# Performance work log

Hardware: AMD Instinct MI355X
Metric: run time of the kernel (lower is better)

The kernel has to match this reference:

```python
import jax, jax.numpy as jnp
import numpy as np

EPS = 1e-5


def _whiten(X, T):
    # X: (B, C, H, W); group whitening with g=1, d=C, m=B*H*W
    B, C, H, W = X.shape
    g, d = 1, C
    x = jnp.transpose(X, (1, 0, 2, 3)).reshape(g, d, -1)  # (g, d, m)
    m = x.shape[-1]
    mean = jnp.mean(x, axis=-1, keepdims=True)
    xc = x - mean
    I = jnp.broadcast_to(jnp.eye(d, dtype=X.dtype)[None], (g, d, d))
    Sigma = EPS * I + jnp.einsum('gim,gjm->gij', xc, xc) / m
    rTr = 1.0 / jnp.trace(Sigma, axis1=1, axis2=2)[:, None, None]  # 1/tr(Sigma)
    Sigma_N = Sigma * rTr
    P = I
    for _ in range(T):  # Newton-Schulz: P <- 1.5*P - 0.5*P^3 @ Sigma_N
        P = 1.5 * P - 0.5 * (P @ P @ P @ Sigma_N)
    wm = P * jnp.sqrt(rTr)  # inverse sqrt of Sigma
    xn = jnp.einsum('gij,gjm->gim', wm, xc)  # (g, d, m)
    return jnp.transpose(xn.reshape(C, B, H, W), (1, 0, 2, 3))


def reference(X, rot, T):
    # mode = -1: whiten then rotate with running_rot, affine=False
    B, C, H, W = X.shape
    g = rot.shape[0]
    d = C // g
    Xn = _whiten(X, T)                       # (B, C, H, W)
    Xh = Xn.reshape(B, g, d, H, W)
    Xr = jnp.einsum('bgchw,gdc->bgdhw', Xh, rot)
    return Xr.reshape(B, C, H, W)


def setup_inputs() -> dict:
    key = jax.random.key(0)
    k1, k2 = jax.random.split(key)
    X = jax.random.normal(k1, (32, 512, 56, 56), dtype=jnp.float32)
    # running_rot buffer; use a random orthogonal matrix for realism
    A = jax.random.normal(k2, (512, 512), dtype=jnp.float32)
    Q, _ = jnp.linalg.qr(A)
    rot = Q[None]  # (1, 512, 512)
    return {"X": X, "rot": rot, "T": 10}
```

## Files before the change

kernel.cpp:

```cpp
#include <hip/hip_runtime.h>
#include <hip/hip_bf16.h>

typedef __bf16 v8bf __attribute__((ext_vector_type(8)));
typedef float  v4f  __attribute__((ext_vector_type(4)));
typedef unsigned short u16;
typedef unsigned int   u32;

#define GAS __attribute__((address_space(1)))
#define LAS __attribute__((address_space(3)))

constexpr int C_ = 512;
constexpr int S_ = 3136;
constexpr int B_ = 32;
constexpr int M_ = B_ * S_;
constexpr float INV_M = 1.0f / (float)M_;

__device__ __forceinline__ void async16(const u16* g, u16* l) {
  __builtin_amdgcn_global_load_lds((const GAS u32*)g, (LAS u32*)l, 16, 0, 0);
}

__device__ __forceinline__ u16 f2bf(float f) {
  u32 u = __builtin_bit_cast(u32, f);
  u += 0x7fffu + ((u >> 16) & 1u);
  return (u16)(u >> 16);
}

__global__ __launch_bounds__(256) void prep_kernel(const float* __restrict__ X,
        u16* __restrict__ xbf, u16* __restrict__ xbfT, float* __restrict__ chsum) {
  __shared__ u16 Ts[64 * 65];
  const int tid = threadIdx.x;
  const int s0 = blockIdx.x * 64;
  const int c0 = blockIdx.y * 64;
  const int b  = blockIdx.z;

  const int i  = tid >> 2;
  const int jc = (tid & 3) * 16;
  const float* xp = X + (b * C_ + c0 + i) * S_ + s0 + jc;
  u16* op = xbf + (c0 + i) * M_ + b * S_ + s0 + jc;
  float ssum = 0.f;
  #pragma unroll
  for (int u = 0; u < 4; ++u) {
    float4 xv = *(const float4*)(xp + u * 4);
    ssum += xv.x + xv.y + xv.z + xv.w;
    u16 e0 = f2bf(xv.x), e1 = f2bf(xv.y), e2 = f2bf(xv.z), e3 = f2bf(xv.w);
    *(ushort4*)(op + u * 4) = make_ushort4(e0, e1, e2, e3);
    const int lb = i * 65 + jc + u * 4;
    Ts[lb + 0] = e0; Ts[lb + 1] = e1; Ts[lb + 2] = e2; Ts[lb + 3] = e3;
  }
  ssum += __shfl_down(ssum, 2, 4);
  ssum += __shfl_down(ssum, 1, 4);
  if ((tid & 3) == 0) atomicAdd(&chsum[c0 + i], ssum);
  __syncthreads();

  const int lane = tid & 63, wv = tid >> 6;
  #pragma unroll
  for (int p = 0; p < 2; ++p) {
    const int j  = p * 32 + wv * 8 + (lane >> 3);
    const int cc = (lane & 7) * 8;
    u16 tmp[8];
    #pragma unroll
    for (int e = 0; e < 8; ++e) tmp[e] = Ts[(cc + e) * 65 + j];
    u16* tp = xbfT + (b * S_ + s0 + j) * C_ + c0 + cc;
    *(ushort4*)(tp + 0) = make_ushort4(tmp[0], tmp[1], tmp[2], tmp[3]);
    *(ushort4*)(tp + 4) = make_ushort4(tmp[4], tmp[5], tmp[6], tmp[7]);
  }
}

__global__ __launch_bounds__(256, 2) void sigma_gemm(const u16* __restrict__ xbf,
                                                     float* __restrict__ part) {
  __shared__ u16 As[128 * 64];
  __shared__ u16 Bs[128 * 64];
  const int tid = threadIdx.x;
  const int tj = blockIdx.x, ti = blockIdx.y, z = blockIdx.z;
  const int kbase = z * S_;
  const int srow = tid >> 3;
  const int scol = (tid & 7) * 8;
  const int lane = tid & 63, wv = tid >> 6;
  const int wm = (wv & 1) * 64, wn = (wv >> 1) * 64;
  const int lr = lane & 15, lq = lane >> 4;
  const u16* gA = xbf + (ti * 128) * M_ + kbase + scol;
  const u16* gB = xbf + (tj * 128) * M_ + kbase + scol;
  v4f acc[4][4] = {};
  for (int it = 0; it < 49; ++it) {
    const int k0 = it * 64;
    #pragma unroll
    for (int q = 0; q < 4; ++q) {
      const int r = q * 32 + srow;
      async16(gA + r * M_ + k0, &As[r * 64 + scol]);
      async16(gB + r * M_ + k0, &Bs[r * 64 + scol]);
    }
    __syncthreads();
    #pragma unroll
    for (int kk = 0; kk < 2; ++kk) {
      v8bf a[4], b[4];
      #pragma unroll
      for (int x = 0; x < 4; ++x) a[x] = *(const v8bf*)&As[(wm + x*16 + lr)*64 + kk*32 + lq*8];
      #pragma unroll
      for (int x = 0; x < 4; ++x) b[x] = *(const v8bf*)&Bs[(wn + x*16 + lr)*64 + kk*32 + lq*8];
      #pragma unroll
      for (int mi = 0; mi < 4; ++mi)
        #pragma unroll
        for (int ni = 0; ni < 4; ++ni)
          acc[mi][ni] = __builtin_amdgcn_mfma_f32_16x16x32_bf16(a[mi], b[ni], acc[mi][ni], 0, 0, 0);
    }
    __syncthreads();
  }
  float* op = part + z * (C_ * C_);
  #pragma unroll
  for (int mi = 0; mi < 4; ++mi) {
    const int gi = ti * 128 + wm + mi * 16 + lq * 4;
    #pragma unroll
    for (int ni = 0; ni < 4; ++ni) {
      const int gj = tj * 128 + wn + ni * 16 + lr;
      #pragma unroll
      for (int r = 0; r < 4; ++r)
        op[(gi + r) * C_ + gj] = acc[mi][ni][r];
    }
  }
}

__global__ __launch_bounds__(256) void reduce_sigma(const float* __restrict__ part,
        const float* __restrict__ chsum, float* __restrict__ Sigma,
        float* __restrict__ trace) {
  const int idx = blockIdx.x * 256 + threadIdx.x;
  const int i = idx >> 9, j = idx & 511;
  float s = 0.f;
  #pragma unroll 8
  for (int z = 0; z < 32; ++z) s += part[z * (C_ * C_) + idx];
  float val = s * INV_M - (chsum[i] * INV_M) * (chsum[j] * INV_M);
  if (i == j) val += 1e-5f;
  Sigma[idx] = val;
  if (i == j) atomicAdd(trace, val);
}

__global__ __launch_bounds__(256) void init_ns(const float* __restrict__ Sigma,
        const float* __restrict__ trace, float* __restrict__ SN, float* __restrict__ P) {
  const int idx = blockIdx.x * 256 + threadIdx.x;
  const float rtr = 1.0f / trace[0];
  SN[idx] = Sigma[idx] * rtr;
  P[idx] = ((idx >> 9) == (idx & 511)) ? 1.0f : 0.f;
}

__global__ __launch_bounds__(256) void mm512_kernel(
    const float* __restrict__ A, const float* __restrict__ Bz0, float* __restrict__ Cz0,
    const float* __restrict__ Bz1, float* __restrict__ Cz1,
    float* __restrict__ P, const float* __restrict__ trace, u16* __restrict__ Cbf,
    const int* __restrict__ Tptr, int iter, int mode) {
  if (Tptr && iter >= Tptr[0]) return;
  const float* Bp = (blockIdx.z == 0) ? Bz0 : Bz1;
  float*       Cp = (blockIdx.z == 0) ? Cz0 : Cz1;
  __shared__ float As[32 * 36];
  __shared__ float Bs[32 * 36];
  const int tid = threadIdx.x;
  const int ro = tid >> 3;
  const int co = (tid & 7) * 4;
  const int ti = blockIdx.y * 32, tj = blockIdx.x * 32;
  float a0 = 0.f, a1 = 0.f, a2 = 0.f, a3 = 0.f;
  for (int k0 = 0; k0 < 512; k0 += 32) {
    float4 av = *(const float4*)(A  + (ti + ro) * 512 + k0 + co);
    float4 bv = *(const float4*)(Bp + (k0 + ro) * 512 + tj + co);
    *(float4*)&As[ro * 36 + co] = av;
    *(float4*)&Bs[ro * 36 + co] = bv;
    __syncthreads();
    #pragma unroll
    for (int k = 0; k < 32; ++k) {
      const float a = As[ro * 36 + k];
      const float4 b = *(const float4*)&Bs[k * 36 + co];
      a0 = fmaf(a, b.x, a0); a1 = fmaf(a, b.y, a1);
      a2 = fmaf(a, b.z, a2); a3 = fmaf(a, b.w, a3);
    }
    __syncthreads();
  }
  const int oidx = (ti + ro) * 512 + tj + co;
  if (mode == 0) {
    Cp[oidx + 0] = a0; Cp[oidx + 1] = a1; Cp[oidx + 2] = a2; Cp[oidx + 3] = a3;
  } else if (mode == 1) {
    float4 pv = *(const float4*)(P + oidx);
    pv.x = 1.5f * pv.x - 0.5f * a0;
    pv.y = 1.5f * pv.y - 0.5f * a1;
    pv.z = 1.5f * pv.z - 0.5f * a2;
    pv.w = 1.5f * pv.w - 0.5f * a3;
    *(float4*)(P + oidx) = pv;
  } else {
    const float sc = sqrtf(1.0f / trace[0]);
    a0 *= sc; a1 *= sc; a2 *= sc; a3 *= sc;
    Cp[oidx + 0] = a0; Cp[oidx + 1] = a1; Cp[oidx + 2] = a2; Cp[oidx + 3] = a3;
    *(ushort4*)(Cbf + oidx) = make_ushort4(f2bf(a0), f2bf(a1), f2bf(a2), f2bf(a3));
  }
}

__global__ __launch_bounds__(256) void calc_v(const float* __restrict__ M2f,
        const float* __restrict__ chsum, float* __restrict__ v) {
  const int d = blockIdx.x * 256 + threadIdx.x;
  float s = 0.f;
  for (int c = 0; c < 512; ++c) s += M2f[d * 512 + c] * (chsum[c] * INV_M);
  v[d] = s;
}

__global__ __launch_bounds__(256, 2) void out_gemm(const u16* __restrict__ Abf,
        const u16* __restrict__ Bt, const float* __restrict__ v, float* __restrict__ out) {
  __shared__ u16 As[128 * 64];
  __shared__ u16 Bs[128 * 64];
  const int tid = threadIdx.x;
  const int tn = blockIdx.x, td = blockIdx.y;
  const int srow = tid >> 3, scol = (tid & 7) * 8;
  const int lane = tid & 63, wv = tid >> 6;
  const int wm = (wv & 1) * 64, wn = (wv >> 1) * 64;
  const int lr = lane & 15, lq = lane >> 4;
  const u16* gA = Abf + (td * 128) * 512 + scol;
  const u16* gB = Bt + (tn * 128) * 512 + scol;
  v4f acc[4][4] = {};
  for (int it = 0; it < 8; ++it) {
    const int k0 = it * 64;
    #pragma unroll
    for (int q = 0; q < 4; ++q) {
      const int r = q * 32 + srow;
      async16(gA + r * 512 + k0, &As[r * 64 + scol]);
      async16(gB + r * 512 + k0, &Bs[r * 64 + scol]);
    }
    __syncthreads();
    #pragma unroll
    for (int kk = 0; kk < 2; ++kk) {
      v8bf a[4], b[4];
      #pragma unroll
      for (int x = 0; x < 4; ++x) a[x] = *(const v8bf*)&As[(wm + x*16 + lr)*64 + kk*32 + lq*8];
      #pragma unroll
      for (int x = 0; x < 4; ++x) b[x] = *(const v8bf*)&Bs[(wn + x*16 + lr)*64 + kk*32 + lq*8];
      #pragma unroll
      for (int mi = 0; mi < 4; ++mi)
        #pragma unroll
        for (int ni = 0; ni < 4; ++ni)
          acc[mi][ni] = __builtin_amdgcn_mfma_f32_16x16x32_bf16(a[mi], b[ni], acc[mi][ni], 0, 0, 0);
    }
    __syncthreads();
  }
  #pragma unroll
  for (int mi = 0; mi < 4; ++mi) {
    const int d0 = td * 128 + wm + mi * 16 + lq * 4;
    const float vd0 = v[d0 + 0], vd1 = v[d0 + 1], vd2 = v[d0 + 2], vd3 = v[d0 + 3];
    #pragma unroll
    for (int ni = 0; ni < 4; ++ni) {
      const unsigned mcol = tn * 128 + wn + ni * 16 + lr;
      const unsigned bb = mcol / 3136u;
      const unsigned ss = mcol - bb * 3136u;
      const int obase = (int)(bb * 512u) * 3136 + (int)ss;
      out[obase + (d0 + 0) * 3136] = acc[mi][ni][0] - vd0;
      out[obase + (d0 + 1) * 3136] = acc[mi][ni][1] - vd1;
      out[obase + (d0 + 2) * 3136] = acc[mi][ni][2] - vd2;
      out[obase + (d0 + 3) * 3136] = acc[mi][ni][3] - vd3;
    }
  }
}

extern "C" void kernel_launch(void* const* d_in, const int* in_sizes, int n_in,
                              void* d_out, int out_size, void* d_ws, size_t ws_size,
                              hipStream_t stream) {
  const float* X   = (const float*)d_in[0];
  const float* rot = (const float*)d_in[1];
  const int*   T   = (const int*)d_in[2];
  float* out = (float*)d_out;

  char* ws = (char*)d_ws;
  size_t off = 0;
  auto alloc = [&](size_t bytes) -> char* {
    char* p = ws + off;
    off += (bytes + 255) & ~(size_t)255;
    return p;
  };
  u16*   xbf   = (u16*)alloc((size_t)C_ * M_ * 2);
  u16*   xbfT  = (u16*)alloc((size_t)M_ * C_ * 2);
  float* part  = (float*)alloc((size_t)32 * C_ * C_ * 4);
  float* Sigma = (float*)alloc((size_t)C_ * C_ * 4);
  float* SN    = (float*)alloc((size_t)C_ * C_ * 4);
  float* P     = (float*)alloc((size_t)C_ * C_ * 4);
  float* T1    = (float*)alloc((size_t)C_ * C_ * 4);
  float* T2    = (float*)alloc((size_t)C_ * C_ * 4);
  float* M2f   = (float*)alloc((size_t)C_ * C_ * 4);
  u16*   M2bf  = (u16*)alloc((size_t)C_ * C_ * 2);
  float* chsum = (float*)alloc(2048);
  float* trace = (float*)alloc(256);
  float* v     = (float*)alloc(2048);
  (void)ws_size; (void)in_sizes; (void)n_in; (void)out_size;

  hipMemsetAsync(chsum, 0, 2048 + 256, stream);

  prep_kernel<<<dim3(49, 8, 32), 256, 0, stream>>>(X, xbf, xbfT, chsum);
  sigma_gemm<<<dim3(4, 4, 32), 256, 0, stream>>>(xbf, part);
  reduce_sigma<<<dim3(1024), 256, 0, stream>>>(part, chsum, Sigma, trace);
  init_ns<<<dim3(1024), 256, 0, stream>>>(Sigma, trace, SN, P);

  for (int iter = 0; iter < 10; ++iter) {
    mm512_kernel<<<dim3(16, 16, 2), 256, 0, stream>>>(P, P, T1, SN, T2, P, trace, M2bf, T, iter, 0);
    mm512_kernel<<<dim3(16, 16, 1), 256, 0, stream>>>(T1, T2, T1, T2, T1, P, trace, M2bf, T, iter, 1);
  }
  mm512_kernel<<<dim3(16, 16, 1), 256, 0, stream>>>(rot, P, M2f, P, M2f, P, trace, M2bf, nullptr, 0, 2);
  calc_v<<<dim3(2), 256, 0, stream>>>(M2f, chsum, v);
  out_gemm<<<dim3(784, 4), 256, 0, stream>>>(M2bf, xbfT, v, out);
}
```

Before: 908.1 us.

## Exploit Sigma symmetry in covariance GEMM and use split-bf16 MFMA for Newton-Schulz

The covariance GEMM now computes only the 10 upper-triangular 128x128 tiles instead of all 16, and the reduction mirrors each value into both halves of Sigma. The Newton-Schulz 512x512 matmuls move from scalar FP32 FMA to MFMA bf16 using a hi/lo split (three MFMAs per product) to keep near-FP32 accuracy. The rot matrix is also pre-split in init. The ns_mm kernel relies on operands being symmetric (B is read by rows, effectively as a transpose), which holds for P, Sigma_N and products of them. That assumption adds some numerical and correctness risk, for example on the final rot·P product.

```diff
diff --git a/kernel.cpp b/kernel.cpp
--- a/kernel.cpp
+++ b/kernel.cpp
@@ -23,6 +23,10 @@
   u32 u = __builtin_bit_cast(u32, f);
   u += 0x7fffu + ((u >> 16) & 1u);
   return (u16)(u >> 16);
+}
+__device__ __forceinline__ float bf2f(u16 h) {
+  u32 u = ((u32)h) << 16;
+  return __builtin_bit_cast(float, u);
 }
 
 __global__ __launch_bounds__(256) void prep_kernel(const float* __restrict__ X,
@@ -71,7 +75,12 @@
   __shared__ u16 As[128 * 64];
   __shared__ u16 Bs[128 * 64];
   const int tid = threadIdx.x;
-  const int tj = blockIdx.x, ti = blockIdx.y, z = blockIdx.z;
+  const int bid = blockIdx.x;
+  const int z = bid & 31;
+  const int t = bid >> 5;
+  const int ti = (t >= 9) ? 3 : (t >= 7) ? 2 : (t >= 4) ? 1 : 0;
+  const int tb = (t >= 9) ? 9 : (t >= 7) ? 7 : (t >= 4) ? 4 : 0;
+  const int tj = ti + (t - tb);
   const int kbase = z * S_;
   const int srow = tid >> 3;
   const int scol = (tid & 7) * 8;
@@ -105,16 +114,16 @@
     }
     __syncthreads();
   }
-  float* op = part + z * (C_ * C_);
+  float* op = part + (size_t)(z * 10 + t) * (128 * 128);
   #pragma unroll
   for (int mi = 0; mi < 4; ++mi) {
-    const int gi = ti * 128 + wm + mi * 16 + lq * 4;
+    const int li = wm + mi * 16 + lq * 4;
     #pragma unroll
     for (int ni = 0; ni < 4; ++ni) {
-      const int gj = tj * 128 + wn + ni * 16 + lr;
+      const int lj = wn + ni * 16 + lr;
       #pragma unroll
       for (int r = 0; r < 4; ++r)
-        op[(gi + r) * C_ + gj] = acc[mi][ni][r];
+        op[(li + r) * 128 + lj] = acc[mi][ni][r];
     }
   }
 }
@@ -123,69 +132,134 @@
         const float* __restrict__ chsum, float* __restrict__ Sigma,
         float* __restrict__ trace) {
   const int idx = blockIdx.x * 256 + threadIdx.x;
-  const int i = idx >> 9, j = idx & 511;
+  const int t = idx >> 14;
+  const int r = idx & 16383;
+  const int ii = r >> 7, jj = r & 127;
+  const int ti = (t >= 9) ? 3 : (t >= 7) ? 2 : (t >= 4) ? 1 : 0;
+  const int tb = (t >= 9) ? 9 : (t >= 7) ? 7 : (t >= 4) ? 4 : 0;
+  const int tj = ti + (t - tb);
+  const int i = ti * 128 + ii, j = tj * 128 + jj;
   float s = 0.f;
   #pragma unroll 8
-  for (int z = 0; z < 32; ++z) s += part[z * (C_ * C_) + idx];
+  for (int z = 0; z < 32; ++z) s += part[(size_t)(z * 10 + t) * 16384 + r];
   float val = s * INV_M - (chsum[i] * INV_M) * (chsum[j] * INV_M);
   if (i == j) val += 1e-5f;
-  Sigma[idx] = val;
+  Sigma[i * 512 + j] = val;
+  if (i != j) Sigma[j * 512 + i] = val;
   if (i == j) atomicAdd(trace, val);
 }
 
 __global__ __launch_bounds__(256) void init_ns(const float* __restrict__ Sigma,
-        const float* __restrict__ trace, float* __restrict__ SN, float* __restrict__ P) {
+        const float* __restrict__ trace, const float* __restrict__ rot,
+        u16* __restrict__ SNhi, u16* __restrict__ SNlo,
+        float* __restrict__ P, u16* __restrict__ Phi, u16* __restrict__ Plo,
+        u16* __restrict__ rothi, u16* __restrict__ rotlo) {
   const int idx = blockIdx.x * 256 + threadIdx.x;
   const float rtr = 1.0f / trace[0];
-  SN[idx] = Sigma[idx] * rtr;
-  P[idx] = ((idx >> 9) == (idx & 511)) ? 1.0f : 0.f;
-}
-
-__global__ __launch_bounds__(256) void mm512_kernel(
-    const float* __restrict__ A, const float* __restrict__ Bz0, float* __restrict__ Cz0,
-    const float* __restrict__ Bz1, float* __restrict__ Cz1,
-    float* __restrict__ P, const float* __restrict__ trace, u16* __restrict__ Cbf,
+  const float sn = Sigma[idx] * rtr;
+  u16 h = f2bf(sn);
+  SNhi[idx] = h; SNlo[idx] = f2bf(sn - bf2f(h));
+  const bool diag = (idx >> 9) == (idx & 511);
+  P[idx] = diag ? 1.0f : 0.f;
+  Phi[idx] = diag ? (u16)0x3F80 : (u16)0;
+  Plo[idx] = 0;
+  const float rv = rot[idx];
+  u16 rh = f2bf(rv);
+  rothi[idx] = rh; rotlo[idx] = f2bf(rv - bf2f(rh));
+}
+
+__global__ __launch_bounds__(256) void ns_mm(
+    const u16* __restrict__ Ahi, const u16* __restrict__ Alo,
+    const u16* __restrict__ B0hi, const u16* __restrict__ B0lo,
+    const u16* __restrict__ B1hi, const u16* __restrict__ B1lo,
+    u16* __restrict__ C0hi, u16* __restrict__ C0lo,
+    u16* __restrict__ C1hi, u16* __restrict__ C1lo,
+    float* __restrict__ P, const float* __restrict__ trace,
+    float* __restrict__ M2f, u16* __restrict__ M2bf,
     const int* __restrict__ Tptr, int iter, int mode) {
   if (Tptr && iter >= Tptr[0]) return;
-  const float* Bp = (blockIdx.z == 0) ? Bz0 : Bz1;
-  float*       Cp = (blockIdx.z == 0) ? Cz0 : Cz1;
-  __shared__ float As[32 * 36];
-  __shared__ float Bs[32 * 36];
+  __shared__ u16 Ah[64 * 64];
+  __shared__ u16 Al[64 * 64];
+  __shared__ u16 Bh[64 * 64];
+  __shared__ u16 Bl[64 * 64];
   const int tid = threadIdx.x;
-  const int ro = tid >> 3;
-  const int co = (tid & 7) * 4;
-  const int ti = blockIdx.y * 32, tj = blockIdx.x * 32;
-  float a0 = 0.f, a1 = 0.f, a2 = 0.f, a3 = 0.f;
-  for (int k0 = 0; k0 < 512; k0 += 32) {
-    float4 av = *(const float4*)(A  + (ti + ro) * 512 + k0 + co);
-    float4 bv = *(const float4*)(Bp + (k0 + ro) * 512 + tj + co);
-    *(float4*)&As[ro * 36 + co] = av;
-    *(float4*)&Bs[ro * 36 + co] = bv;
-    __syncthreads();
-    #pragma unroll
-    for (int k = 0; k < 32; ++k) {
-      const float a = As[ro * 36 + k];
-      const float4 b = *(const float4*)&Bs[k * 36 + co];
-      a0 = fmaf(a, b.x, a0); a1 = fmaf(a, b.y, a1);
-      a2 = fmaf(a, b.z, a2); a3 = fmaf(a, b.w, a3);
-    }
-    __syncthreads();
-  }
-  const int oidx = (ti + ro) * 512 + tj + co;
-  if (mode == 0) {
-    Cp[oidx + 0] = a0; Cp[oidx + 1] = a1; Cp[oidx + 2] = a2; Cp[oidx + 3] = a3;
-  } else if (mode == 1) {
-    float4 pv = *(const float4*)(P + oidx);
-    pv.x = 1.5f * pv.x - 0.5f * a0;
-    pv.y = 1.5f * pv.y - 0.5f * a1;
-    pv.z = 1.5f * pv.z - 0.5f * a2;
-    pv.w = 1.5f * pv.w - 0.5f * a3;
-    *(float4*)(P + oidx) = pv;
-  } else {
-    const float sc = sqrtf(1.0f / trace[0]);
-    a0 *= sc; a1 *= sc; a2 *= sc; a3 *= sc;
-    Cp[oidx + 0] = a0; Cp[oidx + 1] = a1; Cp[oidx + 2] = a2; Cp[oidx + 3] = a3;
-    *(ushort4*)(Cbf + oidx) = make_ushort4(f2bf(a0), f2bf(a1), f2bf(a2), f2bf(a3));
+  const int tj = blockIdx.x, ti = blockIdx.y, zb = blockIdx.z;
+  const u16* Bhip = zb ? B1hi : B0hi;
+  const u16* Blop = zb ? B1lo : B0lo;
+  const int r  = tid >> 3;
+  const int sg = tid & 7;
+  const int swz = (sg ^ (r & 7)) * 8;
+  const int lofs = r * 64 + sg * 8;
+  const u16* gAh = Ahi  + (ti * 64 + r) * 512 + swz;
+  const u16* gAl = Alo  + (ti * 64 + r) * 512 + swz;
+  const u16* gBh = Bhip + (tj * 64 + r) * 512 + swz;
+  const u16* gBl = Blop + (tj * 64 + r) * 512 + swz;
+  const int lane = tid & 63, wv = tid >> 6;
+  const int wr = wv >> 1, wc = wv & 1;
+  const int lr = lane & 15, lq = lane >> 4;
+  v4f acc[2][2] = {};
+  for (int it = 0; it < 8; ++it) {
+    const int k0 = it * 64;
+    async16(gAh + k0,            &Ah[lofs]);
+    async16(gAh + k0 + 32 * 512, &Ah[lofs + 32 * 64]);
+    async16(gAl + k0,            &Al[lofs]);
+    async16(gAl + k0 + 32 * 512, &Al[lofs + 32 * 64]);
+    async16(gBh + k0,            &Bh[lofs]);
+    async16(gBh + k0 + 32 * 512, &Bh[lofs + 32 * 64]);
+    async16(gBl + k0,            &Bl[lofs]);
+    async16(gBl + k0 + 32 * 512, &Bl[lofs + 32 * 64]);
+    __syncthreads();
+    #pragma unroll
+    for (int kk = 0; kk < 2; ++kk) {
+      v8bf ah[2], al[2], bh[2], bl[2];
+      const int col = ((kk * 4 + lq) ^ (lr & 7)) * 8;
+      #pragma unroll
+      for (int x = 0; x < 2; ++x) {
+        const int rowA = (wr * 32 + x * 16 + lr) * 64;
+        ah[x] = *(const v8bf*)&Ah[rowA + col];
+        al[x] = *(const v8bf*)&Al[rowA + col];
+        const int rowB = (wc * 32 + x * 16 + lr) * 64;
+        bh[x] = *(const v8bf*)&Bh[rowB + col];
+        bl[x] = *(const v8bf*)&Bl[rowB + col];
+      }
+      #pragma unroll
+      for (int mi = 0; mi < 2; ++mi)
+        #pragma unroll
+        for (int ni = 0; ni < 2; ++ni) {
+          acc[mi][ni] = __builtin_amdgcn_mfma_f32_16x16x32_bf16(ah[mi], bh[ni], acc[mi][ni], 0, 0, 0);
+          acc[mi][ni] = __builtin_amdgcn_mfma_f32_16x16x32_bf16(ah[mi], bl[ni], acc[mi][ni], 0, 0, 0);
+          acc[mi][ni] = __builtin_amdgcn_mfma_f32_16x16x32_bf16(al[mi], bh[ni], acc[mi][ni], 0, 0, 0);
+        }
+    }
+    __syncthreads();
+  }
+  u16* Chi = zb ? C1hi : C0hi;
+  u16* Clo = zb ? C1lo : C0lo;
+  const float sc = (mode == 2) ? sqrtf(1.0f / trace[0]) : 0.f;
+  #pragma unroll
+  for (int mi = 0; mi < 2; ++mi) {
+    const int gr0 = ti * 64 + wr * 32 + mi * 16 + lq * 4;
+    #pragma unroll
+    for (int ni = 0; ni < 2; ++ni) {
+      const int gc = tj * 64 + wc * 32 + ni * 16 + lr;
+      #pragma unroll
+      for (int q = 0; q < 4; ++q) {
+        const int o = (gr0 + q) * 512 + gc;
+        const float vv = acc[mi][ni][q];
+        if (mode == 0) {
+          u16 h = f2bf(vv);
+          Chi[o] = h; Clo[o] = f2bf(vv - bf2f(h));
+        } else if (mode == 1) {
+          const float nv = 1.5f * P[o] - 0.5f * vv;
+          P[o] = nv;
+          u16 h = f2bf(nv);
+          Chi[o] = h; Clo[o] = f2bf(nv - bf2f(h));
+        } else {
+          const float w = vv * sc;
+          M2f[o] = w; M2bf[o] = f2bf(w);
+        }
+      }
+    }
   }
 }
 
@@ -269,13 +343,20 @@
   };
   u16*   xbf   = (u16*)alloc((size_t)C_ * M_ * 2);
   u16*   xbfT  = (u16*)alloc((size_t)M_ * C_ * 2);
-  float* part  = (float*)alloc((size_t)32 * C_ * C_ * 4);
+  float* part  = (float*)alloc((size_t)320 * 16384 * 4);
   float* Sigma = (float*)alloc((size_t)C_ * C_ * 4);
-  float* SN    = (float*)alloc((size_t)C_ * C_ * 4);
   float* P     = (float*)alloc((size_t)C_ * C_ * 4);
-  float* T1    = (float*)alloc((size_t)C_ * C_ * 4);
-  float* T2    = (float*)alloc((size_t)C_ * C_ * 4);
   float* M2f   = (float*)alloc((size_t)C_ * C_ * 4);
+  u16*   SNhi  = (u16*)alloc((size_t)C_ * C_ * 2);
+  u16*   SNlo  = (u16*)alloc((size_t)C_ * C_ * 2);
+  u16*   Phi   = (u16*)alloc((size_t)C_ * C_ * 2);
+  u16*   Plo   = (u16*)alloc((size_t)C_ * C_ * 2);
+  u16*   T1hi  = (u16*)alloc((size_t)C_ * C_ * 2);
+  u16*   T1lo  = (u16*)alloc((size_t)C_ * C_ * 2);
+  u16*   T2hi  = (u16*)alloc((size_t)C_ * C_ * 2);
+  u16*   T2lo  = (u16*)alloc((size_t)C_ * C_ * 2);
+  u16*   rothi = (u16*)alloc((size_t)C_ * C_ * 2);
+  u16*   rotlo = (u16*)alloc((size_t)C_ * C_ * 2);
   u16*   M2bf  = (u16*)alloc((size_t)C_ * C_ * 2);
   float* chsum = (float*)alloc(2048);
   float* trace = (float*)alloc(256);
@@ -285,15 +366,18 @@
   hipMemsetAsync(chsum, 0, 2048 + 256, stream);
 
   prep_kernel<<<dim3(49, 8, 32), 256, 0, stream>>>(X, xbf, xbfT, chsum);
-  sigma_gemm<<<dim3(4, 4, 32), 256, 0, stream>>>(xbf, part);
-  reduce_sigma<<<dim3(1024), 256, 0, stream>>>(part, chsum, Sigma, trace);
-  init_ns<<<dim3(1024), 256, 0, stream>>>(Sigma, trace, SN, P);
+  sigma_gemm<<<dim3(320), 256, 0, stream>>>(xbf, part);
+  reduce_sigma<<<dim3(640), 256, 0, stream>>>(part, chsum, Sigma, trace);
+  init_ns<<<dim3(1024), 256, 0, stream>>>(Sigma, trace, rot, SNhi, SNlo, P, Phi, Plo, rothi, rotlo);
 
   for (int iter = 0; iter < 10; ++iter) {
-    mm512_kernel<<<dim3(16, 16, 2), 256, 0, stream>>>(P, P, T1, SN, T2, P, trace, M2bf, T, iter, 0);
-    mm512_kernel<<<dim3(16, 16, 1), 256, 0, stream>>>(T1, T2, T1, T2, T1, P, trace, M2bf, T, iter, 1);
-  }
-  mm512_kernel<<<dim3(16, 16, 1), 256, 0, stream>>>(rot, P, M2f, P, M2f, P, trace, M2bf, nullptr, 0, 2);
+    ns_mm<<<dim3(8, 8, 2), 256, 0, stream>>>(Phi, Plo, Phi, Plo, SNhi, SNlo,
+        T1hi, T1lo, T2hi, T2lo, P, trace, M2f, M2bf, T, iter, 0);
+    ns_mm<<<dim3(8, 8, 1), 256, 0, stream>>>(T1hi, T1lo, T2hi, T2lo, nullptr, nullptr,
+        Phi, Plo, nullptr, nullptr, P, trace, M2f, M2bf, T, iter, 1);
+  }
+  ns_mm<<<dim3(8, 8, 1), 256, 0, stream>>>(rothi, rotlo, Phi, Plo, nullptr, nullptr,
+      Phi, Plo, nullptr, nullptr, P, trace, M2f, M2bf, nullptr, 0, 2);
   calc_v<<<dim3(2), 256, 0, stream>>>(M2f, chsum, v);
   out_gemm<<<dim3(784, 4), 256, 0, stream>>>(M2bf, xbfT, v, out);
 }
```

Result: faster. 805.0 us (-11.4%).
